# Performance work log

Measured on AMD Instinct MI355X. Metric: run time of the kernel, lower is better.

The kernel has to match this reference:

```python
import jax, jax.numpy as jnp
import numpy as np

B, H, N = 2, 4, 8192
K = 32       # sub_size
TEMP = 2.0   # temperature for the soft permutation indicator


def setup_inputs() -> dict:
    key = jax.random.key(0)
    ranking = jax.random.normal(key, (B, H, N, 1), dtype=jnp.float32)
    return {"ranking": ranking, "i": 0, "j": N}


@jax.custom_vjp
def hsigmoid(x):
    # Hard step indicator (x > 0) with straight-through gradient (CoCN Hsigmoid)
    return (x > 0).astype(x.dtype)

def _hs_fwd(x):
    return hsigmoid(x), None

def _hs_bwd(res, g):
    return (g,)

hsigmoid.defvjp(_hs_fwd, _hs_bwd)


def _windows(x, n, k):
    # circular pad last dim by k-1, then unfold into sliding windows of size k
    xp = jnp.concatenate([x, x[..., :k - 1]], axis=-1)
    idx = jnp.arange(n)[:, None] + jnp.arange(k)[None, :]   # (n, k)
    return xp[..., idx]                                      # (..., n, k)


def reference(ranking, i, j):
    b, h, n = ranking.shape[:3]
    k = K
    r = ranking[..., 0]                                      # (b,h,n)
    order = jnp.argsort(r, axis=2, stable=True)              # (b,h,n) stable sort indices
    r_sorted = jnp.take_along_axis(r, order, axis=2)

    val_win = _windows(r_sorted, n, k)                       # (b,h,n,k)
    idx_win = _windows(order.astype(jnp.float32), n, k).astype(jnp.int32)

    # scatter windows back to original node order == gather by inverse permutation
    inv = jnp.argsort(order, axis=2)                         # (b,h,n)
    val_win = jnp.take_along_axis(val_win, inv[..., None], axis=2)
    idx_win = jnp.take_along_axis(idx_win, inv[..., None], axis=2)

    # within each window, sort by original node index (stable), reorder values alike
    k_order = jnp.argsort(idx_win, axis=-1, stable=True)
    sorted_idx = jnp.take_along_axis(idx_win, k_order, axis=-1)
    val_win = jnp.take_along_axis(val_win, k_order, axis=-1)

    # slice node window [i, i+j)
    val_win = val_win[:, :, i:i + j]                         # (b,h,j,k)
    sorted_idx = sorted_idx[:, :, i:i + j]

    # (b,j,h,k) -> (b*j, h, k, 1)
    x = jnp.transpose(val_win, (0, 2, 1, 3)).reshape(-1, h, k, 1)
    rel = x - jnp.swapaxes(x, -1, -2)                        # (b*j,h,k,k)
    tie_bias = jnp.triu((rel == 0).astype(jnp.float32), 1)   # break ties above diagonal
    rel = rel + tie_bias
    uni = hsigmoid(jax.nn.relu(rel))                         # 1 where strictly greater
    rank = jnp.sum(uni, axis=-2, keepdims=True)              # (b*j,h,1,k)

    ind = jnp.arange(k, dtype=jnp.float32)[:, None] - rank   # (b*j,h,k,k)
    ind = jnp.where(ind < 0, ind + k, ind)
    perm = jnp.exp(-ind * TEMP)
    return perm, sorted_idx
```

## Files before the change

### kernel.cpp

```cpp
#include <hip/hip_runtime.h>
#include <stdint.h>

#define B_ 2
#define H_ 4
#define N_ 8192
#define K_ 32
#define ROWS (B_ * H_)
#define PERM_ELEMS ((size_t)B_ * N_ * H_ * K_ * K_)

__global__ __launch_bounds__(1024) void sort_rows(
    const float* __restrict__ ranking,
    float* __restrict__ r_sorted,
    int* __restrict__ order,
    int* __restrict__ inv)
{
    __shared__ uint64_t keys[N_];
    const int row = blockIdx.x;
    const float* r = ranking + (size_t)row * N_;

    for (int i = threadIdx.x; i < N_; i += blockDim.x) {
        uint32_t u = __float_as_uint(r[i]);
        u = (u & 0x80000000u) ? ~u : (u | 0x80000000u);
        keys[i] = ((uint64_t)u << 32) | (uint32_t)i;
    }
    __syncthreads();

    for (int kk = 2; kk <= N_; kk <<= 1) {
        for (int jj = kk >> 1; jj > 0; jj >>= 1) {
            for (int i = threadIdx.x; i < N_; i += blockDim.x) {
                int ixj = i ^ jj;
                if (ixj > i) {
                    uint64_t a = keys[i];
                    uint64_t b = keys[ixj];
                    bool up = ((i & kk) == 0);
                    if ((a > b) == up) { keys[i] = b; keys[ixj] = a; }
                }
            }
            __syncthreads();
        }
    }

    for (int s = threadIdx.x; s < N_; s += blockDim.x) {
        uint64_t kv = keys[s];
        uint32_t e = (uint32_t)(kv >> 32);
        uint32_t idx = (uint32_t)kv;
        uint32_t u = (e & 0x80000000u) ? (e & 0x7FFFFFFFu) : ~e;
        r_sorted[(size_t)row * N_ + s] = __uint_as_float(u);
        order[(size_t)row * N_ + s] = (int)idx;
        inv[(size_t)row * N_ + idx] = s;
    }
}

__global__ __launch_bounds__(256) void windows_kernel(
    const float* __restrict__ r_sorted,
    const int* __restrict__ order,
    const int* __restrict__ inv,
    float* __restrict__ perm_out,
    float* __restrict__ idx_out)
{
    __shared__ float etab[K_];
    __shared__ int lds_id[8][K_];
    __shared__ int lds_rank[8][K_];

    const int tid = threadIdx.x;
    if (tid < K_) etab[tid] = expf(-2.0f * (float)tid);

    const int wave  = tid >> 6;
    const int lane  = tid & 63;
    const int half  = lane >> 5;
    const int m     = lane & 31;
    const int wslot = wave * 2 + half;

    const long w  = (long)blockIdx.x * 8 + wslot;
    const int row = (int)(w >> 13);
    const int n   = (int)(w & (N_ - 1));

    const float* rs = r_sorted + (size_t)row * N_;
    const int*   od = order + (size_t)row * N_;

    const int t = inv[(size_t)row * N_ + n];
    int g = t + m; if (g >= N_) g -= N_;
    const float v = rs[g];
    const int  id = od[g];

    int rank = 0, pos = 0;
    #pragma unroll
    for (int p = 0; p < K_; ++p) {
        float vv = __shfl(v, p, 32);
        int   ii = __shfl(id, p, 32);
        rank += (vv > v) || (vv == v && ii < id);
        pos  += (ii < id);
    }

    lds_id[wslot][pos]   = id;
    lds_rank[wslot][pos] = rank;
    __syncthreads();

    const int b = row >> 2;
    const int h = row & 3;

    const size_t idx_base = (((size_t)(b * H_ + h)) * N_ + n) * K_;
    idx_out[idx_base + m] = (float)lds_id[wslot][m];

    float4* pout = (float4*)(perm_out + (((size_t)b * N_ + n) * H_ + h) * (K_ * K_));
    #pragma unroll
    for (int q = 0; q < 8; ++q) {
        const int f4 = q * 32 + m;
        const int mm = f4 >> 3;
        const int j0 = (f4 & 7) * 4;
        float4 val;
        val.x = etab[(mm - lds_rank[wslot][j0 + 0]) & 31];
        val.y = etab[(mm - lds_rank[wslot][j0 + 1]) & 31];
        val.z = etab[(mm - lds_rank[wslot][j0 + 2]) & 31];
        val.w = etab[(mm - lds_rank[wslot][j0 + 3]) & 31];
        pout[f4] = val;
    }
}

extern "C" void kernel_launch(void* const* d_in, const int* in_sizes, int n_in,
                              void* d_out, int out_size, void* d_ws, size_t ws_size,
                              hipStream_t stream) {
    const float* ranking = (const float*)d_in[0];

    float* ws = (float*)d_ws;
    float* r_sorted = ws;
    int*   order    = (int*)(ws + (size_t)ROWS * N_);
    int*   inv      = (int*)(ws + (size_t)2 * ROWS * N_);

    float* perm_out = (float*)d_out;
    float* idx_out  = perm_out + PERM_ELEMS;

    hipLaunchKernelGGL(sort_rows, dim3(ROWS), dim3(1024), 0, stream,
                       ranking, r_sorted, order, inv);
    hipLaunchKernelGGL(windows_kernel, dim3((B_ * H_ * N_) / 8), dim3(256), 0, stream,
                       r_sorted, order, inv, perm_out, idx_out);
}
```

Baseline: 385.4 us.

## Replace per-row bitonic sort with parallel rank-counting sort and scatter

```diff
diff --git a/kernel.cpp b/kernel.cpp
--- a/kernel.cpp
+++ b/kernel.cpp
@@ -5,114 +5,142 @@
 #define H_ 4
 #define N_ 8192
 #define K_ 32
-#define ROWS (B_ * H_)
+#define ROWS 8
+#define NTOT (ROWS * N_)
 #define PERM_ELEMS ((size_t)B_ * N_ * H_ * K_ * K_)
 
-__global__ __launch_bounds__(1024) void sort_rows(
-    const float* __restrict__ ranking,
-    float* __restrict__ r_sorted,
-    int* __restrict__ order,
-    int* __restrict__ inv)
-{
-    __shared__ uint64_t keys[N_];
-    const int row = blockIdx.x;
-    const float* r = ranking + (size_t)row * N_;
+__global__ __launch_bounds__(256) void pack_keys(const float* __restrict__ ranking,
+                                                 uint64_t* __restrict__ keys,
+                                                 int* __restrict__ rank) {
+    const int g = blockIdx.x * 256 + threadIdx.x;
+    uint32_t u = __float_as_uint(ranking[g]);
+    u = (u & 0x80000000u) ? ~u : (u | 0x80000000u);
+    keys[g] = ((uint64_t)u << 13) | (uint32_t)(g & (N_ - 1));
+    rank[g] = 0;
+}
 
-    for (int i = threadIdx.x; i < N_; i += blockDim.x) {
-        uint32_t u = __float_as_uint(r[i]);
-        u = (u & 0x80000000u) ? ~u : (u | 0x80000000u);
-        keys[i] = ((uint64_t)u << 32) | (uint32_t)i;
-    }
+#define JT 1024
+#define IT 2048
+#define EPT 8
+
+__global__ __launch_bounds__(256) void rank_count(const uint64_t* __restrict__ keys,
+                                                  int* __restrict__ rank) {
+    __shared__ uint64_t jk[JT];
+    const int blk = blockIdx.x;
+    const int jt  = blk & 7;
+    const int it  = (blk >> 3) & 3;
+    const int row = blk >> 5;
+    const uint64_t* rk = keys + (size_t)row * N_;
+
+    for (int j = threadIdx.x; j < JT; j += 256)
+        jk[j] = rk[jt * JT + j];
+
+    uint64_t my[EPT];
+    const int ibase = it * IT + threadIdx.x;
+    #pragma unroll
+    for (int e = 0; e < EPT; ++e) my[e] = rk[ibase + e * 256];
     __syncthreads();
 
-    for (int kk = 2; kk <= N_; kk <<= 1) {
-        for (int jj = kk >> 1; jj > 0; jj >>= 1) {
-            for (int i = threadIdx.x; i < N_; i += blockDim.x) {
-                int ixj = i ^ jj;
-                if (ixj > i) {
-                    uint64_t a = keys[i];
-                    uint64_t b = keys[ixj];
-                    bool up = ((i & kk) == 0);
-                    if ((a > b) == up) { keys[i] = b; keys[ixj] = a; }
-                }
-            }
-            __syncthreads();
+    int cnt[EPT] = {0, 0, 0, 0, 0, 0, 0, 0};
+    for (int j = 0; j < JT; j += 2) {
+        const uint64_t k0 = jk[j];
+        const uint64_t k1 = jk[j + 1];
+        #pragma unroll
+        for (int e = 0; e < EPT; ++e) {
+            cnt[e] += (k0 < my[e]);
+            cnt[e] += (k1 < my[e]);
         }
     }
+    #pragma unroll
+    for (int e = 0; e < EPT; ++e)
+        atomicAdd(&rank[(size_t)row * N_ + ibase + e * 256], cnt[e]);
+}
 
-    for (int s = threadIdx.x; s < N_; s += blockDim.x) {
-        uint64_t kv = keys[s];
-        uint32_t e = (uint32_t)(kv >> 32);
-        uint32_t idx = (uint32_t)kv;
-        uint32_t u = (e & 0x80000000u) ? (e & 0x7FFFFFFFu) : ~e;
-        r_sorted[(size_t)row * N_ + s] = __uint_as_float(u);
-        order[(size_t)row * N_ + s] = (int)idx;
-        inv[(size_t)row * N_ + idx] = s;
-    }
+__global__ __launch_bounds__(256) void scatter_sorted(const float* __restrict__ ranking,
+                                                      const int* __restrict__ rank,
+                                                      int2* __restrict__ vid,
+                                                      int* __restrict__ inv) {
+    const int g = blockIdx.x * 256 + threadIdx.x;
+    const int row = g >> 13;
+    const int s = rank[g];
+    inv[g] = s;
+    vid[(size_t)row * N_ + s] = make_int2(__float_as_int(ranking[g]), g & (N_ - 1));
 }
 
 __global__ __launch_bounds__(256) void windows_kernel(
-    const float* __restrict__ r_sorted,
-    const int* __restrict__ order,
+    const int2* __restrict__ vid,
     const int* __restrict__ inv,
     float* __restrict__ perm_out,
     float* __restrict__ idx_out)
 {
-    __shared__ float etab[K_];
-    __shared__ int lds_id[8][K_];
-    __shared__ int lds_rank[8][K_];
+    __shared__ float etabN[K_];
+    __shared__ float etabP[K_];
+    __shared__ uint64_t wk[8][K_];
+    __shared__ float2 cinfo[8][K_ + 1];
+    __shared__ float idf[8][K_];
 
     const int tid = threadIdx.x;
-    if (tid < K_) etab[tid] = expf(-2.0f * (float)tid);
+    if (tid < K_) {
+        etabN[tid] = expf(-2.0f * (float)tid);
+        etabP[tid] = expf(2.0f * (float)tid);
+    }
 
-    const int wave  = tid >> 6;
-    const int lane  = tid & 63;
-    const int half  = lane >> 5;
-    const int m     = lane & 31;
-    const int wslot = wave * 2 + half;
+    const int wave = tid >> 6;
+    const int lane = tid & 63;
+    const int half = lane >> 5;
+    const int m    = lane & 31;
+    const int ws   = wave * 2 + half;
 
-    const long w  = (long)blockIdx.x * 8 + wslot;
-    const int row = (int)(w >> 13);
-    const int n   = (int)(w & (N_ - 1));
-
-    const float* rs = r_sorted + (size_t)row * N_;
-    const int*   od = order + (size_t)row * N_;
+    const int w   = blockIdx.x * 8 + ws;
+    const int row = w >> 13;
+    const int n   = w & (N_ - 1);
 
     const int t = inv[(size_t)row * N_ + n];
     int g = t + m; if (g >= N_) g -= N_;
-    const float v = rs[g];
-    const int  id = od[g];
+    const int2 vi = vid[(size_t)row * N_ + g];
+    const int id = vi.y;
+    uint32_t u = (uint32_t)vi.x;
+    u = (u & 0x80000000u) ? ~u : (u | 0x80000000u);
+    const int rid = (N_ - 1) - id;
+    const uint64_t key2 = ((uint64_t)u << 13) | (uint32_t)rid;
+
+    wk[ws][m] = key2;
+    __syncthreads();
 
     int rank = 0, pos = 0;
     #pragma unroll
     for (int p = 0; p < K_; ++p) {
-        float vv = __shfl(v, p, 32);
-        int   ii = __shfl(id, p, 32);
-        rank += (vv > v) || (vv == v && ii < id);
-        pos  += (ii < id);
+        const uint64_t kp = wk[ws][p];
+        rank += (kp > key2);
+        pos  += ((int)((uint32_t)kp & (uint32_t)(N_ - 1)) > rid);
     }
 
-    lds_id[wslot][pos]   = id;
-    lds_rank[wslot][pos] = rank;
+    cinfo[ws][pos] = make_float2(etabP[rank], __int_as_float(rank));
+    idf[ws][pos]   = (float)id;
     __syncthreads();
+
+    idx_out[((size_t)row * N_ + n) * K_ + m] = idf[ws][m];
 
     const int b = row >> 2;
     const int h = row & 3;
+    float4* pout = (float4*)(perm_out + (((size_t)b * N_ + n) * H_ + h) * (K_ * K_));
+    const float E64C = 1.6038108e-28f;
 
-    const size_t idx_base = (((size_t)(b * H_ + h)) * N_ + n) * K_;
-    idx_out[idx_base + m] = (float)lds_id[wslot][m];
-
-    float4* pout = (float4*)(perm_out + (((size_t)b * N_ + n) * H_ + h) * (K_ * K_));
     #pragma unroll
     for (int q = 0; q < 8; ++q) {
         const int f4 = q * 32 + m;
         const int mm = f4 >> 3;
         const int j0 = (f4 & 7) * 4;
+        const float a = etabN[mm];
+        const float2 c0 = cinfo[ws][j0 + 0];
+        const float2 c1 = cinfo[ws][j0 + 1];
+        const float2 c2 = cinfo[ws][j0 + 2];
+        const float2 c3 = cinfo[ws][j0 + 3];
         float4 val;
-        val.x = etab[(mm - lds_rank[wslot][j0 + 0]) & 31];
-        val.y = etab[(mm - lds_rank[wslot][j0 + 1]) & 31];
-        val.z = etab[(mm - lds_rank[wslot][j0 + 2]) & 31];
-        val.w = etab[(mm - lds_rank[wslot][j0 + 3]) & 31];
+        val.x = a * c0.x * (mm < __float_as_int(c0.y) ? E64C : 1.0f);
+        val.y = a * c1.x * (mm < __float_as_int(c1.y) ? E64C : 1.0f);
+        val.z = a * c2.x * (mm < __float_as_int(c2.y) ? E64C : 1.0f);
+        val.w = a * c3.x * (mm < __float_as_int(c3.y) ? E64C : 1.0f);
         pout[f4] = val;
     }
 }
@@ -122,16 +150,21 @@
                               hipStream_t stream) {
     const float* ranking = (const float*)d_in[0];
 
-    float* ws = (float*)d_ws;
-    float* r_sorted = ws;
-    int*   order    = (int*)(ws + (size_t)ROWS * N_);
-    int*   inv      = (int*)(ws + (size_t)2 * ROWS * N_);
+    char* ws = (char*)d_ws;
+    uint64_t* keys = (uint64_t*)ws;
+    int*      rank = (int*)(ws + 512 * 1024);
+    int2*     vid  = (int2*)(ws + 768 * 1024);
+    int*      inv  = (int*)(ws + 1280 * 1024);
 
     float* perm_out = (float*)d_out;
     float* idx_out  = perm_out + PERM_ELEMS;
 
-    hipLaunchKernelGGL(sort_rows, dim3(ROWS), dim3(1024), 0, stream,
-                       ranking, r_sorted, order, inv);
-    hipLaunchKernelGGL(windows_kernel, dim3((B_ * H_ * N_) / 8), dim3(256), 0, stream,
-                       r_sorted, order, inv, perm_out, idx_out);
+    hipLaunchKernelGGL(pack_keys, dim3(NTOT / 256), dim3(256), 0, stream,
+                       ranking, keys, rank);
+    hipLaunchKernelGGL(rank_count, dim3(256), dim3(256), 0, stream,
+                       keys, rank);
+    hipLaunchKernelGGL(scatter_sorted, dim3(NTOT / 256), dim3(256), 0, stream,
+                       ranking, rank, vid, inv);
+    hipLaunchKernelGGL(windows_kernel, dim3((ROWS * N_) / 8), dim3(256), 0, stream,
+                       vid, inv, perm_out, idx_out);
 }
```

Result: faster. 318.2 us (-17.4%).
